# Performance work log

Hardware: AMD Instinct MI355X
Metric: run time of the kernel (lower is better)

The kernel has to match this reference:

```python
import jax, jax.numpy as jnp
import numpy as np

N_NODES = 100000
N_EDGES = 3200000
IN_DIM, HID, LAT = 81, 64, 32
BN_EPS = 1e-5


def setup_inputs() -> dict:
    key = jax.random.key(0)
    ks = jax.random.split(key, 16)
    def w(k, fan_in, fan_out):
        lim = 1.0 / np.sqrt(fan_in)
        return jax.random.uniform(k, (fan_in, fan_out), jnp.float32, -lim, lim)
    inp = {
        "x": jax.random.normal(ks[0], (N_NODES, IN_DIM), jnp.float32),
        "edge_index": jax.random.randint(ks[1], (2, N_EDGES), 0, N_NODES, jnp.int64),
        "W1": w(ks[2], IN_DIM, HID), "b1": jnp.zeros((HID,), jnp.float32),
        "g1": jnp.ones((HID,), jnp.float32), "beta1": jnp.zeros((HID,), jnp.float32),
        "W2": w(ks[3], HID, HID), "b2": jnp.zeros((HID,), jnp.float32),
        "g2": jnp.ones((HID,), jnp.float32), "beta2": jnp.zeros((HID,), jnp.float32),
        "Wmu": w(ks[4], HID, LAT), "bmu": jnp.zeros((LAT,), jnp.float32),
        "Wls": w(ks[5], HID, LAT), "bls": jnp.zeros((LAT,), jnp.float32),
    }
    return inp


def _gcn_norm(edge_index, num_nodes):
    # PyG gcn_norm: add self-loops, symmetric D^-1/2 A D^-1/2
    loop = jnp.arange(num_nodes, dtype=edge_index.dtype)
    src = jnp.concatenate([edge_index[0], loop])
    dst = jnp.concatenate([edge_index[1], loop])
    deg = jax.ops.segment_sum(jnp.ones_like(src, dtype=jnp.float32), dst,
                              num_segments=num_nodes)
    dis = jnp.where(deg > 0, jax.lax.rsqrt(jnp.maximum(deg, 1.0)), 0.0)
    norm = dis[src] * dis[dst]  # [E + N]
    return src, dst, norm


def _gcn_conv(x, W, b, src, dst, norm, num_nodes):
    h = x @ W                          # [N, out]
    msg = h[src] * norm[:, None]       # gather + scale
    out = jax.ops.segment_sum(msg, dst, num_segments=num_nodes)  # scatter-add
    return out + b


def _batchnorm(h, g, beta):
    m = h.mean(axis=0)
    v = h.var(axis=0)  # biased, as torch uses for normalization
    return (h - m) * jax.lax.rsqrt(v + BN_EPS) * g + beta


def reference(x, edge_index, W1, b1, g1, beta1, W2, b2, g2, beta2,
              Wmu, bmu, Wls, bls):
    n = x.shape[0]
    src, dst, norm = _gcn_norm(edge_index, n)
    h = _gcn_conv(x, W1, b1, src, dst, norm, n)
    h = jax.nn.relu(_batchnorm(h, g1, beta1))  # dropout = identity (eval)
    h = _gcn_conv(h, W2, b2, src, dst, norm, n)
    h = jax.nn.relu(_batchnorm(h, g2, beta2))
    mu = _gcn_conv(h, Wmu, bmu, src, dst, norm, n)
    logstd = _gcn_conv(h, Wls, bls, src, dst, norm, n)
    return (mu, logstd)
```

## Files before the change

### kernel.cpp

```cpp
#include <hip/hip_runtime.h>
#include <stdint.h>

#define N_NODES 100000
#define N_EDGES 3200000
#define IN_DIM  81
#define HID     64
#define LAT     32
#define BN_EPS  1e-5f
#define NBUCKET 391
#define EPB     8192
#define NBLK_E  391

__device__ __forceinline__ float bfu2f(unsigned short u) {
    return __uint_as_float(((uint32_t)u) << 16);
}
__device__ __forceinline__ unsigned short f2bfu(float f) {
    uint32_t x = __float_as_uint(f);
    return (unsigned short)((x + 0x7FFFu + ((x >> 16) & 1u)) >> 16);
}
__device__ __forceinline__ float loadf(const void* p, size_t i, int fp32) {
    if (fp32) return ((const float*)p)[i];
    return bfu2f(((const unsigned short*)p)[i]);
}
__device__ __forceinline__ int load_dst(const void* ei, int f64, long e) {
    if (f64) return (int)(((const long long*)ei)[(size_t)N_EDGES + e]);
    return ((const int*)ei)[(size_t)N_EDGES + e];
}
__device__ __forceinline__ int load_src(const void* ei, int f64, long e) {
    if (f64) return (int)(((const long long*)ei)[e]);
    return ((const int*)ei)[e];
}
__device__ __forceinline__ float bcast(float v, int k) {
    return __int_as_float(__builtin_amdgcn_readlane(__float_as_int(v), k));
}

__device__ __forceinline__ void fma8(float* acc, uint4 v, float d) {
    acc[0] = fmaf(__uint_as_float(v.x << 16), d, acc[0]);
    acc[1] = fmaf(__uint_as_float(v.x & 0xffff0000u), d, acc[1]);
    acc[2] = fmaf(__uint_as_float(v.y << 16), d, acc[2]);
    acc[3] = fmaf(__uint_as_float(v.y & 0xffff0000u), d, acc[3]);
    acc[4] = fmaf(__uint_as_float(v.z << 16), d, acc[4]);
    acc[5] = fmaf(__uint_as_float(v.z & 0xffff0000u), d, acc[5]);
    acc[6] = fmaf(__uint_as_float(v.w << 16), d, acc[6]);
    acc[7] = fmaf(__uint_as_float(v.w & 0xffff0000u), d, acc[7]);
}

__global__ void stamp_kernel(float* out, int n, float v) {
    int i = blockIdx.x * blockDim.x + threadIdx.x;
    if (i < n) out[i] = v;
}

__global__ void detect_all(const int* ei_raw,
                           const void* x, const void* W1, const void* b1,
                           const void* g1, const void* be1, const void* W2,
                           const void* b2, const void* g2, const void* be2,
                           const void* Wmu, const void* bmu, const void* Wls,
                           const void* bls, int* flags,
                           float* stats, int* bcnt) {
    int w = threadIdx.x >> 6;
    int lane = threadIdx.x & 63;
    if (w == 14) {
        for (int i = lane; i < 256; i += 64) stats[i] = 0.0f;
        return;
    }
    if (w == 15) {
        for (int i = lane; i < NBUCKET; i += 64) bcnt[i] = 0;
        return;
    }
    if (w == 13) {
        int acc = ei_raw[2 * lane * 11003 + 1] |
                  ei_raw[2 * (lane + 64) * 11003 + 1];
        unsigned long long b = __ballot(acc != 0);
        if (lane == 0) flags[0] = (b == 0ull) ? 1 : 0;
        return;
    }
    const void* bufs[13] = { x, W1, b1, g1, be1, W2, b2, g2, be2, Wmu, bmu, Wls, bls };
    const int   ns[13]   = { 512, 512, 64, 64, 64, 512, 64, 64, 64, 512, 32, 512, 32 };
    const unsigned short* u = (const unsigned short*)bufs[w];
    int n = ns[w];
    int evenZero = 0;
    bool oddNz = false, anyNz = false, big = false;
    for (int i = lane; i < n; i += 64) {
        unsigned short s = u[i];
        if (s) anyNz = true;
        if (i & 1) { if (s) oddNz = true; }
        else {
            if ((s & 0x7F80u) == 0x7F80u) big = true;
            else if (fabsf(bfu2f(s)) > 100.0f) big = true;
            if (s == 0) evenZero++;
        }
    }
    unsigned long long anyB = __ballot(anyNz);
    unsigned long long oddB = __ballot(oddNz);
    unsigned long long bigB = __ballot(big);
#pragma unroll
    for (int o = 1; o < 64; o <<= 1) evenZero += __shfl_xor(evenZero, o);
    if (lane == 0) {
        int fp32 = 0;
        if (anyB != 0ull) {
            if (bigB != 0ull) fp32 = 1;
            else if (evenZero >= n / 4 && oddB != 0ull) fp32 = 1;
        }
        flags[1 + w] = fp32;
    }
}

__global__ void convert_weights(const void* W1, const void* W2,
                                const void* Wmu, const void* Wls,
                                const void* b1, const void* b2,
                                const void* bmu, const void* bls,
                                const int* flags,
                                float* W1f, float* W2f, float* Wcatf,
                                float* b1f, float* b2f, float* bcatf) {
    int i = blockIdx.x * blockDim.x + threadIdx.x;
    if (i < IN_DIM * HID) { W1f[i] = loadf(W1, i, flags[2]); return; }
    i -= IN_DIM * HID;
    if (i < HID * HID) { W2f[i] = loadf(W2, i, flags[6]); return; }
    i -= HID * HID;
    if (i < HID * HID) {
        int k = i >> 6;
        int j = i & 63;
        if (j < LAT) Wcatf[i] = loadf(Wmu, (size_t)k * LAT + j, flags[10]);
        else         Wcatf[i] = loadf(Wls, (size_t)k * LAT + (j - LAT), flags[12]);
        return;
    }
    i -= HID * HID;
    if (i < HID) { b1f[i] = loadf(b1, i, flags[3]); return; }
    i -= HID;
    if (i < HID) { b2f[i] = loadf(b2, i, flags[7]); return; }
    i -= HID;
    if (i < HID) {
        if (i < LAT) bcatf[i] = loadf(bmu, i, flags[11]);
        else         bcatf[i] = loadf(bls, i - LAT, flags[13]);
    }
}

__global__ void bucket_hist(const void* ei, const int* flags, int* bcnt) {
    __shared__ int h[NBUCKET];
    for (int i = threadIdx.x; i < NBUCKET; i += 256) h[i] = 0;
    __syncthreads();
    int f64 = flags[0];
    long e0 = (long)blockIdx.x * EPB;
    for (int i = 0; i < EPB / 256; i++) {
        long e = e0 + i * 256 + threadIdx.x;
        if (e < N_EDGES) atomicAdd(&h[load_dst(ei, f64, e) >> 8], 1);
    }
    __syncthreads();
    for (int i = threadIdx.x; i < NBUCKET; i += 256)
        if (h[i]) atomicAdd(&bcnt[i], h[i]);
}

__global__ void bucket_scan(const int* bcnt, int* bbase, int* bcur, int* row_start) {
    __shared__ int sd[512];
    int t = threadIdx.x;
    int v0 = (t < NBUCKET) ? bcnt[t] : 0;
    int v1 = (t + 256 < NBUCKET) ? bcnt[t + 256] : 0;
    sd[t] = v0;
    sd[t + 256] = v1;
    __syncthreads();
    for (int off = 1; off < 256; off <<= 1) {
        int x = (t >= off) ? sd[t - off] : 0;
        __syncthreads();
        sd[t] += x;
        __syncthreads();
    }
    int low_total = sd[255];
    for (int off = 1; off < 256; off <<= 1) {
        int x = (t >= off) ? sd[256 + t - off] : 0;
        __syncthreads();
        sd[256 + t] += x;
        __syncthreads();
    }
    if (t < NBUCKET) {
        int excl = sd[t] - v0;
        bbase[t] = excl;
        bcur[t] = excl;
    }
    int j = 256 + t;
    if (j < NBUCKET) {
        int excl = sd[j] + low_total - v1;
        bbase[j] = excl;
        bcur[j] = excl;
    }
    if (t == 0) {
        bbase[NBUCKET] = N_EDGES;
        row_start[N_NODES] = N_EDGES;
    }
}

__global__ void bucket_scatter(const void* ei, const int* flags, int* bcur,
                               int* staged) {
    __shared__ int h[NBUCKET];
    __shared__ int lbase[NBUCKET];
    __shared__ int cnt[NBUCKET];
    for (int i = threadIdx.x; i < NBUCKET; i += 256) { h[i] = 0; cnt[i] = 0; }
    __syncthreads();
    int f64 = flags[0];
    long e0 = (long)blockIdx.x * EPB;
    for (int i = 0; i < EPB / 256; i++) {
        long e = e0 + i * 256 + threadIdx.x;
        if (e < N_EDGES) atomicAdd(&h[load_dst(ei, f64, e) >> 8], 1);
    }
    __syncthreads();
    for (int i = threadIdx.x; i < NBUCKET; i += 256)
        lbase[i] = h[i] ? atomicAdd(&bcur[i], h[i]) : 0;
    __syncthreads();
    for (int i = 0; i < EPB / 256; i++) {
        long e = e0 + i * 256 + threadIdx.x;
        if (e < N_EDGES) {
            int d = load_dst(ei, f64, e);
            int s = load_src(ei, f64, e);
            int b = d >> 8;
            int off = atomicAdd(&cnt[b], 1);
            staged[lbase[b] + off] = ((d & 255) << 17) | s;
        }
    }
}

__global__ void csr_build(const int* bbase, const int* staged, float* dis,
                          int* row_start, int* csr) {
    int b = blockIdx.x;
    int t = threadIdx.x;
    int n0 = b << 8;
    int nn = N_NODES - n0;
    if (nn > 256) nn = 256;
    int e0 = bbase[b];
    int e1 = bbase[b + 1];
    __shared__ int ldeg[256];
    __shared__ int lcur[256];
    __shared__ int sd[256];
    ldeg[t] = 0;
    __syncthreads();
    for (int i = e0 + t; i < e1; i += 256)
        atomicAdd(&ldeg[staged[i] >> 17], 1);
    __syncthreads();
    int v = ldeg[t];
    sd[t] = v;
    __syncthreads();
    for (int off = 1; off < 256; off <<= 1) {
        int x = (t >= off) ? sd[t - off] : 0;
        __syncthreads();
        sd[t] += x;
        __syncthreads();
    }
    int excl = sd[t] - v;
    if (t < nn) {
        dis[n0 + t] = rsqrtf((float)(v + 1));
        row_start[n0 + t] = e0 + excl;
    }
    lcur[t] = e0 + excl;
    __syncthreads();
    for (int i = e0 + t; i < e1; i += 256) {
        int rec = staged[i];
        int pos = atomicAdd(&lcur[rec >> 17], 1);
        csr[pos] = rec & 0x1FFFF;
    }
}

__global__ void gemm_l1(const void* X, const int* flags, const float* W,
                        unsigned short* T) {
    int wid = (blockIdx.x * blockDim.x + threadIdx.x) >> 6;
    int n0 = wid * 4;
    if (n0 >= N_NODES) return;
    int lane = threadIdx.x & 63;
    int fp = flags[1];
    float xa[4], xb[4];
#pragma unroll
    for (int nn = 0; nn < 4; nn++) {
        size_t base = (size_t)(n0 + nn) * IN_DIM;
        xa[nn] = loadf(X, base + lane, fp);
        xb[nn] = (lane < IN_DIM - 64) ? loadf(X, base + 64 + lane, fp) : 0.0f;
    }
    float acc[4] = { 0.0f, 0.0f, 0.0f, 0.0f };
    const float* Wp = W + lane;
#pragma unroll
    for (int k = 0; k < 64; k++) {
        float w = Wp[k * HID];
#pragma unroll
        for (int nn = 0; nn < 4; nn++)
            acc[nn] = fmaf(bcast(xa[nn], k), w, acc[nn]);
    }
#pragma unroll
    for (int k = 0; k < IN_DIM - 64; k++) {
        float w = Wp[(64 + k) * HID];
#pragma unroll
        for (int nn = 0; nn < 4; nn++)
            acc[nn] = fmaf(bcast(xb[nn], k), w, acc[nn]);
    }
#pragma unroll
    for (int nn = 0; nn < 4; nn++)
        T[(size_t)(n0 + nn) * HID + lane] = f2bfu(acc[nn]);
}

__global__ void gemm_bn(const float* F, const float* W,
                        const float* scale, const float* shift, unsigned short* T) {
    int wid = (blockIdx.x * blockDim.x + threadIdx.x) >> 6;
    int n0 = wid * 4;
    if (n0 >= N_NODES) return;
    int lane = threadIdx.x & 63;
    float sc = scale[lane];
    float sh = shift[lane];
    float a[4];
#pragma unroll
    for (int nn = 0; nn < 4; nn++) {
        float f = F[(size_t)(n0 + nn) * HID + lane];
        a[nn] = fmaxf(f * sc + sh, 0.0f);
    }
    float acc[4] = { 0.0f, 0.0f, 0.0f, 0.0f };
    const float* Wp = W + lane;
#pragma unroll
    for (int k = 0; k < HID; k++) {
        float w = Wp[k * HID];
#pragma unroll
        for (int nn = 0; nn < 4; nn++)
            acc[nn] = fmaf(bcast(a[nn], k), w, acc[nn]);
    }
#pragma unroll
    for (int nn = 0; nn < 4; nn++)
        T[(size_t)(n0 + nn) * HID + lane] = f2bfu(acc[nn]);
}

__global__ void agg_mid(const unsigned short* T, const int* row_start, const int* csr,
                        const float* dis, const float* bias, float* F) {
    int wid = (blockIdx.x * blockDim.x + threadIdx.x) >> 6;
    if (wid >= N_NODES) return;
    int lane = threadIdx.x & 63;
    int g = lane >> 3;
    int c = lane & 7;
    float dn = dis[wid];
    float acc[8];
#pragma unroll
    for (int k = 0; k < 8; k++) acc[k] = 0.0f;
    if (g == 0) {
        uint4 v = ((const uint4*)(T + (size_t)wid * HID))[c];
        fma8(acc, v, dn);
    }
    int s0 = row_start[wid];
    int s1 = row_start[wid + 1];
    for (int e = s0; e < s1; e += 32) {
        int i0 = e + g;
        int i1 = e + 8 + g;
        int i2 = e + 16 + g;
        int i3 = e + 24 + g;
        int m0 = i0 < s1, m1 = i1 < s1, m2 = i2 < s1, m3 = i3 < s1;
        int n0i = csr[m0 ? i0 : s0];
        int n1i = csr[m1 ? i1 : s0];
        int n2i = csr[m2 ? i2 : s0];
        int n3i = csr[m3 ? i3 : s0];
        float d0 = m0 ? dis[n0i] : 0.0f;
        float d1 = m1 ? dis[n1i] : 0.0f;
        float d2 = m2 ? dis[n2i] : 0.0f;
        float d3 = m3 ? dis[n3i] : 0.0f;
        uint4 v0 = ((const uint4*)(T + (size_t)n0i * HID))[c];
        uint4 v1 = ((const uint4*)(T + (size_t)n1i * HID))[c];
        uint4 v2 = ((const uint4*)(T + (size_t)n2i * HID))[c];
        uint4 v3 = ((const uint4*)(T + (size_t)n3i * HID))[c];
        fma8(acc, v0, d0);
        fma8(acc, v1, d1);
        fma8(acc, v2, d2);
        fma8(acc, v3, d3);
    }
#pragma unroll
    for (int k = 0; k < 8; k++) {
        float v = acc[k];
        v += __shfl_xor(v, 8);
        v += __shfl_xor(v, 16);
        v += __shfl_xor(v, 32);
        acc[k] = v;
    }
    if (g == 0) {
        const float4* bp = (const float4*)(bias + c * 8);
        float4 b0 = bp[0];
        float4 b1 = bp[1];
        float4 r0, r1;
        r0.x = b0.x + dn * acc[0];
        r0.y = b0.y + dn * acc[1];
        r0.z = b0.z + dn * acc[2];
        r0.w = b0.w + dn * acc[3];
        r1.x = b1.x + dn * acc[4];
        r1.y = b1.y + dn * acc[5];
        r1.z = b1.z + dn * acc[6];
        r1.w = b1.w + dn * acc[7];
        float4* o = (float4*)(F + (size_t)wid * HID + c * 8);
        o[0] = r0;
        o[1] = r1;
    }
}

__global__ void agg_out(const unsigned short* T, const int* row_start, const int* csr,
                        const float* dis, const float* bias, float* out) {
    int wid = (blockIdx.x * blockDim.x + threadIdx.x) >> 6;
    if (wid >= N_NODES) return;
    int lane = threadIdx.x & 63;
    int g = lane >> 3;
    int c = lane & 7;
    float dn = dis[wid];
    float acc[8];
#pragma unroll
    for (int k = 0; k < 8; k++) acc[k] = 0.0f;
    if (g == 0) {
        uint4 v = ((const uint4*)(T + (size_t)wid * HID))[c];
        fma8(acc, v, dn);
    }
    int s0 = row_start[wid];
    int s1 = row_start[wid + 1];
    for (int e = s0; e < s1; e += 32) {
        int i0 = e + g;
        int i1 = e + 8 + g;
        int i2 = e + 16 + g;
        int i3 = e + 24 + g;
        int m0 = i0 < s1, m1 = i1 < s1, m2 = i2 < s1, m3 = i3 < s1;
        int n0i = csr[m0 ? i0 : s0];
        int n1i = csr[m1 ? i1 : s0];
        int n2i = csr[m2 ? i2 : s0];
        int n3i = csr[m3 ? i3 : s0];
        float d0 = m0 ? dis[n0i] : 0.0f;
        float d1 = m1 ? dis[n1i] : 0.0f;
        float d2 = m2 ? dis[n2i] : 0.0f;
        float d3 = m3 ? dis[n3i] : 0.0f;
        uint4 v0 = ((const uint4*)(T + (size_t)n0i * HID))[c];
        uint4 v1 = ((const uint4*)(T + (size_t)n1i * HID))[c];
        uint4 v2 = ((const uint4*)(T + (size_t)n2i * HID))[c];
        uint4 v3 = ((const uint4*)(T + (size_t)n3i * HID))[c];
        fma8(acc, v0, d0);
        fma8(acc, v1, d1);
        fma8(acc, v2, d2);
        fma8(acc, v3, d3);
    }
#pragma unroll
    for (int k = 0; k < 8; k++) {
        float v = acc[k];
        v += __shfl_xor(v, 8);
        v += __shfl_xor(v, 16);
        v += __shfl_xor(v, 32);
        acc[k] = v;
    }
    if (g == 0) {
        const float4* bp = (const float4*)(bias + c * 8);
        float4 b0 = bp[0];
        float4 b1 = bp[1];
        float4 r0, r1;
        r0.x = b0.x + dn * acc[0];
        r0.y = b0.y + dn * acc[1];
        r0.z = b0.z + dn * acc[2];
        r0.w = b0.w + dn * acc[3];
        r1.x = b1.x + dn * acc[4];
        r1.y = b1.y + dn * acc[5];
        r1.z = b1.z + dn * acc[6];
        r1.w = b1.w + dn * acc[7];
        float4* o;
        if (c < 4)
            o = (float4*)(out + (size_t)wid * LAT + c * 8);
        else
            o = (float4*)(out + (size_t)N_NODES * LAT + (size_t)wid * LAT + (c - 4) * 8);
        o[0] = r0;
        o[1] = r1;
    }
}

__global__ void stats_kernel(const float* F, float* stats) {
    int lane = threadIdx.x & 63;
    int wv = threadIdx.x >> 6;
    float s = 0.0f;
    float q = 0.0f;
    for (int r = blockIdx.x * 4 + wv; r < N_NODES; r += gridDim.x * 4) {
        float v = F[(size_t)r * HID + lane];
        s += v;
        q += v * v;
    }
    __shared__ float ls[256];
    __shared__ float lq[256];
    ls[threadIdx.x] = s;
    lq[threadIdx.x] = q;
    __syncthreads();
    if (threadIdx.x < 64) {
        s = ls[threadIdx.x] + ls[64 + threadIdx.x] + ls[128 + threadIdx.x] + ls[192 + threadIdx.x];
        q = lq[threadIdx.x] + lq[64 + threadIdx.x] + lq[128 + threadIdx.x] + lq[192 + threadIdx.x];
        atomicAdd(&stats[lane], s);
        atomicAdd(&stats[64 + lane], q);
    }
}

__global__ void finalize_bn(const float* stats, const void* g, const void* beta,
                            const int* flags, int gflag, int bflag,
                            float* scale, float* shift) {
    int j = threadIdx.x;
    if (j >= HID) return;
    float inv_n = 1.0f / (float)N_NODES;
    float mean = stats[j] * inv_n;
    float var = stats[64 + j] * inv_n - mean * mean;
    float sc = loadf(g, j, flags[gflag]) * rsqrtf(var + BN_EPS);
    scale[j] = sc;
    shift[j] = loadf(beta, j, flags[bflag]) - mean * sc;
}

extern "C" void kernel_launch(void* const* d_in, const int* in_sizes, int n_in,
                              void* d_out, int out_size, void* d_ws, size_t ws_size,
                              hipStream_t stream) {
    (void)in_sizes;
    (void)n_in;
    const void* x   = d_in[0];
    const void* ei  = d_in[1];
    const void* W1  = d_in[2];
    const void* b1  = d_in[3];
    const void* g1  = d_in[4];
    const void* be1 = d_in[5];
    const void* W2  = d_in[6];
    const void* b2  = d_in[7];
    const void* g2  = d_in[8];
    const void* be2 = d_in[9];
    const void* Wmu = d_in[10];
    const void* bmu = d_in[11];
    const void* Wls = d_in[12];
    const void* bls = d_in[13];
    float* out = (float*)d_out;

    char* base = (char*)d_ws;
    size_t off = 0;
    int* staged = (int*)(base + off);
    off += (size_t)N_EDGES * 4;        off = (off + 511) & ~(size_t)511;
    int* csr = (int*)(base + off);
    off += (size_t)N_EDGES * 4;        off = (off + 511) & ~(size_t)511;
    unsigned short* T = (unsigned short*)(base + off);
    off += (size_t)N_NODES * HID * 2;  off = (off + 511) & ~(size_t)511;
    float* F = (float*)(base + off);
    off += (size_t)N_NODES * HID * 4;  off = (off + 511) & ~(size_t)511;
    float* dis = (float*)(base + off);
    off += (size_t)N_NODES * 4;        off = (off + 511) & ~(size_t)511;
    int* row_start = (int*)(base + off);
    off += (size_t)(N_NODES + 1) * 4;  off = (off + 511) & ~(size_t)511;
    int* bcnt = (int*)(base + off);
    off += NBUCKET * 4;                off = (off + 511) & ~(size_t)511;
    int* bbase = (int*)(base + off);
    off += (NBUCKET + 1) * 4;          off = (off + 511) & ~(size_t)511;
    int* bcur = (int*)(base + off);
    off += NBUCKET * 4;                off = (off + 511) & ~(size_t)511;
    int* flags = (int*)(base + off);
    off += 512;                        off = (off + 511) & ~(size_t)511;
    float* W1f = (float*)(base + off);
    off += (size_t)IN_DIM * HID * 4;   off = (off + 511) & ~(size_t)511;
    float* W2f = (float*)(base + off);
    off += (size_t)HID * HID * 4;      off = (off + 511) & ~(size_t)511;
    float* Wcatf = (float*)(base + off);
    off += (size_t)HID * HID * 4;      off = (off + 511) & ~(size_t)511;
    float* b1f = (float*)(base + off);
    off += HID * 4;                    off = (off + 511) & ~(size_t)511;
    float* b2f = (float*)(base + off);
    off += HID * 4;                    off = (off + 511) & ~(size_t)511;
    float* bcatf = (float*)(base + off);
    off += HID * 4;                    off = (off + 511) & ~(size_t)511;
    float* stats = (float*)(base + off);
    off += 256 * 4;                    off = (off + 511) & ~(size_t)511;
    float* scale1 = (float*)(base + off);
    off += HID * 4;                    off = (off + 511) & ~(size_t)511;
    float* shift1 = (float*)(base + off);
    off += HID * 4;                    off = (off + 511) & ~(size_t)511;
    float* scale2 = (float*)(base + off);
    off += HID * 4;                    off = (off + 511) & ~(size_t)511;
    float* shift2 = (float*)(base + off);
    off += HID * 4;

    const int BT = 256;
    int gW   = (N_NODES * 64 + BT - 1) / BT;
    int gG   = ((N_NODES / 4) * 64 + BT - 1) / BT;
    int gOut = (out_size + BT - 1) / BT;
    int gCv  = (IN_DIM * HID + 2 * HID * HID + 3 * HID + BT - 1) / BT;

    if (ws_size < off) {
        stamp_kernel<<<gOut, BT, 0, stream>>>(out, out_size, 6.8e37f);
        return;
    }

    detect_all<<<1, 1024, 0, stream>>>((const int*)ei, x, W1, b1, g1, be1, W2, b2,
                                       g2, be2, Wmu, bmu, Wls, bls, flags,
                                       stats, bcnt);
    convert_weights<<<gCv, BT, 0, stream>>>(W1, W2, Wmu, Wls, b1, b2, bmu, bls,
                                            flags, W1f, W2f, Wcatf, b1f, b2f, bcatf);

    bucket_hist<<<NBLK_E, BT, 0, stream>>>(ei, flags, bcnt);
    bucket_scan<<<1, BT, 0, stream>>>(bcnt, bbase, bcur, row_start);
    bucket_scatter<<<NBLK_E, BT, 0, stream>>>(ei, flags, bcur, staged);
    csr_build<<<NBUCKET, BT, 0, stream>>>(bbase, staged, dis, row_start, csr);

    gemm_l1<<<gG, BT, 0, stream>>>(x, flags, W1f, T);
    agg_mid<<<gW, BT, 0, stream>>>(T, row_start, csr, dis, b1f, F);
    stats_kernel<<<256, BT, 0, stream>>>(F, stats);
    finalize_bn<<<1, 64, 0, stream>>>(stats, g1, be1, flags, 4, 5, scale1, shift1);

    gemm_bn<<<gG, BT, 0, stream>>>(F, W2f, scale1, shift1, T);
    agg_mid<<<gW, BT, 0, stream>>>(T, row_start, csr, dis, b2f, F);
    stats_kernel<<<256, BT, 0, stream>>>(F, stats + 128);
    finalize_bn<<<1, 64, 0, stream>>>(stats + 128, g2, be2, flags, 8, 9, scale2, shift2);

    gemm_bn<<<gG, BT, 0, stream>>>(F, Wcatf, scale2, shift2, T);
    agg_out<<<gW, BT, 0, stream>>>(T, row_start, csr, dis, bcatf, out);
}
```

Before: 541.9 us.

## Fuse BN stats into aggregation and drop histogram/scan passes via fixed-capacity buckets

```diff
diff --git a/kernel.cpp b/kernel.cpp
--- a/kernel.cpp
+++ b/kernel.cpp
@@ -10,6 +10,8 @@
 #define NBUCKET 391
 #define EPB     8192
 #define NBLK_E  391
+#define BCAP    16384
+#define NSLICE  16
 
 __device__ __forceinline__ float bfu2f(unsigned short u) {
     return __uint_as_float(((uint32_t)u) << 16);
@@ -56,15 +58,15 @@
                            const void* b2, const void* g2, const void* be2,
                            const void* Wmu, const void* bmu, const void* Wls,
                            const void* bls, int* flags,
-                           float* stats, int* bcnt) {
+                           float* statsA, float* statsB, int* gcnt) {
     int w = threadIdx.x >> 6;
     int lane = threadIdx.x & 63;
     if (w == 14) {
-        for (int i = lane; i < 256; i += 64) stats[i] = 0.0f;
+        for (int i = lane; i < NSLICE * 128; i += 64) statsA[i] = 0.0f;
         return;
     }
     if (w == 15) {
-        for (int i = lane; i < NBUCKET; i += 64) bcnt[i] = 0;
+        for (int i = lane; i < NSLICE * 128; i += 64) statsB[i] = 0.0f;
         return;
     }
     if (w == 13) {
@@ -72,6 +74,7 @@
                   ei_raw[2 * (lane + 64) * 11003 + 1];
         unsigned long long b = __ballot(acc != 0);
         if (lane == 0) flags[0] = (b == 0ull) ? 1 : 0;
+        for (int i = lane; i < NBUCKET; i += 64) gcnt[i] = 0;
         return;
     }
     const void* bufs[13] = { x, W1, b1, g1, be1, W2, b2, g2, be2, Wmu, bmu, Wls, bls };
@@ -135,9 +138,12 @@
     }
 }
 
-__global__ void bucket_hist(const void* ei, const int* flags, int* bcnt) {
+__global__ void bucket_scatter(const void* ei, const int* flags, int* gcnt,
+                               int* staged) {
     __shared__ int h[NBUCKET];
-    for (int i = threadIdx.x; i < NBUCKET; i += 256) h[i] = 0;
+    __shared__ int lbase[NBUCKET];
+    __shared__ int lcnt[NBUCKET];
+    for (int i = threadIdx.x; i < NBUCKET; i += 256) { h[i] = 0; lcnt[i] = 0; }
     __syncthreads();
     int f64 = flags[0];
     long e0 = (long)blockIdx.x * EPB;
@@ -147,63 +153,7 @@
     }
     __syncthreads();
     for (int i = threadIdx.x; i < NBUCKET; i += 256)
-        if (h[i]) atomicAdd(&bcnt[i], h[i]);
-}
-
-__global__ void bucket_scan(const int* bcnt, int* bbase, int* bcur, int* row_start) {
-    __shared__ int sd[512];
-    int t = threadIdx.x;
-    int v0 = (t < NBUCKET) ? bcnt[t] : 0;
-    int v1 = (t + 256 < NBUCKET) ? bcnt[t + 256] : 0;
-    sd[t] = v0;
-    sd[t + 256] = v1;
-    __syncthreads();
-    for (int off = 1; off < 256; off <<= 1) {
-        int x = (t >= off) ? sd[t - off] : 0;
-        __syncthreads();
-        sd[t] += x;
-        __syncthreads();
-    }
-    int low_total = sd[255];
-    for (int off = 1; off < 256; off <<= 1) {
-        int x = (t >= off) ? sd[256 + t - off] : 0;
-        __syncthreads();
-        sd[256 + t] += x;
-        __syncthreads();
-    }
-    if (t < NBUCKET) {
-        int excl = sd[t] - v0;
-        bbase[t] = excl;
-        bcur[t] = excl;
-    }
-    int j = 256 + t;
-    if (j < NBUCKET) {
-        int excl = sd[j] + low_total - v1;
-        bbase[j] = excl;
-        bcur[j] = excl;
-    }
-    if (t == 0) {
-        bbase[NBUCKET] = N_EDGES;
-        row_start[N_NODES] = N_EDGES;
-    }
-}
-
-__global__ void bucket_scatter(const void* ei, const int* flags, int* bcur,
-                               int* staged) {
-    __shared__ int h[NBUCKET];
-    __shared__ int lbase[NBUCKET];
-    __shared__ int cnt[NBUCKET];
-    for (int i = threadIdx.x; i < NBUCKET; i += 256) { h[i] = 0; cnt[i] = 0; }
-    __syncthreads();
-    int f64 = flags[0];
-    long e0 = (long)blockIdx.x * EPB;
-    for (int i = 0; i < EPB / 256; i++) {
-        long e = e0 + i * 256 + threadIdx.x;
-        if (e < N_EDGES) atomicAdd(&h[load_dst(ei, f64, e) >> 8], 1);
-    }
-    __syncthreads();
-    for (int i = threadIdx.x; i < NBUCKET; i += 256)
-        lbase[i] = h[i] ? atomicAdd(&bcur[i], h[i]) : 0;
+        lbase[i] = h[i] ? atomicAdd(&gcnt[i], h[i]) : 0;
     __syncthreads();
     for (int i = 0; i < EPB / 256; i++) {
         long e = e0 + i * 256 + threadIdx.x;
@@ -211,28 +161,38 @@
             int d = load_dst(ei, f64, e);
             int s = load_src(ei, f64, e);
             int b = d >> 8;
-            int off = atomicAdd(&cnt[b], 1);
-            staged[lbase[b] + off] = ((d & 255) << 17) | s;
-        }
-    }
-}
-
-__global__ void csr_build(const int* bbase, const int* staged, float* dis,
+            int off = atomicAdd(&lcnt[b], 1);
+            staged[(b << 14) + lbase[b] + off] = ((d & 255) << 17) | s;
+        }
+    }
+}
+
+__global__ void csr_build(const int* gcnt, const int* staged, float* dis,
                           int* row_start, int* csr) {
     int b = blockIdx.x;
     int t = threadIdx.x;
     int n0 = b << 8;
     int nn = N_NODES - n0;
     if (nn > 256) nn = 256;
-    int e0 = bbase[b];
-    int e1 = bbase[b + 1];
+    __shared__ int sd[256];
     __shared__ int ldeg[256];
     __shared__ int lcur[256];
-    __shared__ int sd[256];
+    int p = 0;
+    for (int i = t; i < b; i += 256) p += gcnt[i];
+    sd[t] = p;
+    __syncthreads();
+    for (int off = 128; off >= 1; off >>= 1) {
+        if (t < off) sd[t] += sd[t + off];
+        __syncthreads();
+    }
+    int e0 = sd[0];
+    int cntb = gcnt[b];
+    __syncthreads();
     ldeg[t] = 0;
     __syncthreads();
-    for (int i = e0 + t; i < e1; i += 256)
-        atomicAdd(&ldeg[staged[i] >> 17], 1);
+    const int* sb = staged + ((size_t)b << 14);
+    for (int i = t; i < cntb; i += 256)
+        atomicAdd(&ldeg[sb[i] >> 17], 1);
     __syncthreads();
     int v = ldeg[t];
     sd[t] = v;
@@ -250,11 +210,12 @@
     }
     lcur[t] = e0 + excl;
     __syncthreads();
-    for (int i = e0 + t; i < e1; i += 256) {
-        int rec = staged[i];
+    for (int i = t; i < cntb; i += 256) {
+        int rec = sb[i];
         int pos = atomicAdd(&lcur[rec >> 17], 1);
         csr[pos] = rec & 0x1FFFF;
     }
+    if (b == NBUCKET - 1 && t == 0) row_start[N_NODES] = e0 + cntb;
 }
 
 __global__ void gemm_l1(const void* X, const int* flags, const float* W,
@@ -292,14 +253,24 @@
         T[(size_t)(n0 + nn) * HID + lane] = f2bfu(acc[nn]);
 }
 
-__global__ void gemm_bn(const float* F, const float* W,
-                        const float* scale, const float* shift, unsigned short* T) {
+__global__ void gemm_bn(const float* F, const float* W, const float* stats,
+                        const void* gw, const void* bw, const int* flags,
+                        int gf, int bf, unsigned short* T) {
     int wid = (blockIdx.x * blockDim.x + threadIdx.x) >> 6;
     int n0 = wid * 4;
     if (n0 >= N_NODES) return;
     int lane = threadIdx.x & 63;
-    float sc = scale[lane];
-    float sh = shift[lane];
+    float s = 0.0f, q = 0.0f;
+#pragma unroll
+    for (int sl = 0; sl < NSLICE; sl++) {
+        s += stats[sl * 128 + lane];
+        q += stats[sl * 128 + 64 + lane];
+    }
+    const float inv_n = 1.0f / (float)N_NODES;
+    float mean = s * inv_n;
+    float var = q * inv_n - mean * mean;
+    float sc = loadf(gw, lane, flags[gf]) * rsqrtf(var + BN_EPS);
+    float sh = loadf(bw, lane, flags[bf]) - mean * sc;
     float a[4];
 #pragma unroll
     for (int nn = 0; nn < 4; nn++) {
@@ -321,7 +292,94 @@
 }
 
 __global__ void agg_mid(const unsigned short* T, const int* row_start, const int* csr,
-                        const float* dis, const float* bias, float* F) {
+                        const float* dis, const float* bias, float* F, float* stats) {
+    __shared__ float ls[64];
+    __shared__ float lq[64];
+    if (threadIdx.x < 64) { ls[threadIdx.x] = 0.0f; lq[threadIdx.x] = 0.0f; }
+    __syncthreads();
+    int wid = (blockIdx.x * blockDim.x + threadIdx.x) >> 6;
+    int lane = threadIdx.x & 63;
+    int g = lane >> 3;
+    int c = lane & 7;
+    if (wid < N_NODES) {
+        float dn = dis[wid];
+        float acc[8];
+#pragma unroll
+        for (int k = 0; k < 8; k++) acc[k] = 0.0f;
+        if (g == 0) {
+            uint4 v = ((const uint4*)(T + (size_t)wid * HID))[c];
+            fma8(acc, v, dn);
+        }
+        int s0 = row_start[wid];
+        int s1 = row_start[wid + 1];
+        for (int e = s0; e < s1; e += 32) {
+            int i0 = e + g;
+            int i1 = e + 8 + g;
+            int i2 = e + 16 + g;
+            int i3 = e + 24 + g;
+            int m0 = i0 < s1, m1 = i1 < s1, m2 = i2 < s1, m3 = i3 < s1;
+            int n0i = csr[m0 ? i0 : s0];
+            int n1i = csr[m1 ? i1 : s0];
+            int n2i = csr[m2 ? i2 : s0];
+            int n3i = csr[m3 ? i3 : s0];
+            float d0 = m0 ? dis[n0i] : 0.0f;
+            float d1 = m1 ? dis[n1i] : 0.0f;
+            float d2 = m2 ? dis[n2i] : 0.0f;
+            float d3 = m3 ? dis[n3i] : 0.0f;
+            uint4 v0 = ((const uint4*)(T + (size_t)n0i * HID))[c];
+            uint4 v1 = ((const uint4*)(T + (size_t)n1i * HID))[c];
+            uint4 v2 = ((const uint4*)(T + (size_t)n2i * HID))[c];
+            uint4 v3 = ((const uint4*)(T + (size_t)n3i * HID))[c];
+            fma8(acc, v0, d0);
+            fma8(acc, v1, d1);
+            fma8(acc, v2, d2);
+            fma8(acc, v3, d3);
+        }
+#pragma unroll
+        for (int k = 0; k < 8; k++) {
+            float v = acc[k];
+            v += __shfl_xor(v, 8);
+            v += __shfl_xor(v, 16);
+            v += __shfl_xor(v, 32);
+            acc[k] = v;
+        }
+        if (g == 0) {
+            const float4* bp = (const float4*)(bias + c * 8);
+            float4 b0 = bp[0];
+            float4 b1 = bp[1];
+            float4 r0, r1;
+            r0.x = b0.x + dn * acc[0];
+            r0.y = b0.y + dn * acc[1];
+            r0.z = b0.z + dn * acc[2];
+            r0.w = b0.w + dn * acc[3];
+            r1.x = b1.x + dn * acc[4];
+            r1.y = b1.y + dn * acc[5];
+            r1.z = b1.z + dn * acc[6];
+            r1.w = b1.w + dn * acc[7];
+            float4* o = (float4*)(F + (size_t)wid * HID + c * 8);
+            o[0] = r0;
+            o[1] = r1;
+            int f0 = c * 8;
+            atomicAdd(&ls[f0 + 0], r0.x); atomicAdd(&lq[f0 + 0], r0.x * r0.x);
+            atomicAdd(&ls[f0 + 1], r0.y); atomicAdd(&lq[f0 + 1], r0.y * r0.y);
+            atomicAdd(&ls[f0 + 2], r0.z); atomicAdd(&lq[f0 + 2], r0.z * r0.z);
+            atomicAdd(&ls[f0 + 3], r0.w); atomicAdd(&lq[f0 + 3], r0.w * r0.w);
+            atomicAdd(&ls[f0 + 4], r1.x); atomicAdd(&lq[f0 + 4], r1.x * r1.x);
+            atomicAdd(&ls[f0 + 5], r1.y); atomicAdd(&lq[f0 + 5], r1.y * r1.y);
+            atomicAdd(&ls[f0 + 6], r1.z); atomicAdd(&lq[f0 + 6], r1.z * r1.z);
+            atomicAdd(&ls[f0 + 7], r1.w); atomicAdd(&lq[f0 + 7], r1.w * r1.w);
+        }
+    }
+    __syncthreads();
+    if (threadIdx.x < 64) {
+        int sl = blockIdx.x & (NSLICE - 1);
+        atomicAdd(&stats[sl * 128 + threadIdx.x], ls[threadIdx.x]);
+        atomicAdd(&stats[sl * 128 + 64 + threadIdx.x], lq[threadIdx.x]);
+    }
+}
+
+__global__ void agg_out(const unsigned short* T, const int* row_start, const int* csr,
+                        const float* dis, const float* bias, float* out) {
     int wid = (blockIdx.x * blockDim.x + threadIdx.x) >> 6;
     if (wid >= N_NODES) return;
     int lane = threadIdx.x & 63;
@@ -381,73 +439,6 @@
         r1.y = b1.y + dn * acc[5];
         r1.z = b1.z + dn * acc[6];
         r1.w = b1.w + dn * acc[7];
-        float4* o = (float4*)(F + (size_t)wid * HID + c * 8);
-        o[0] = r0;
-        o[1] = r1;
-    }
-}
-
-__global__ void agg_out(const unsigned short* T, const int* row_start, const int* csr,
-                        const float* dis, const float* bias, float* out) {
-    int wid = (blockIdx.x * blockDim.x + threadIdx.x) >> 6;
-    if (wid >= N_NODES) return;
-    int lane = threadIdx.x & 63;
-    int g = lane >> 3;
-    int c = lane & 7;
-    float dn = dis[wid];
-    float acc[8];
-#pragma unroll
-    for (int k = 0; k < 8; k++) acc[k] = 0.0f;
-    if (g == 0) {
-        uint4 v = ((const uint4*)(T + (size_t)wid * HID))[c];
-        fma8(acc, v, dn);
-    }
-    int s0 = row_start[wid];
-    int s1 = row_start[wid + 1];
-    for (int e = s0; e < s1; e += 32) {
-        int i0 = e + g;
-        int i1 = e + 8 + g;
-        int i2 = e + 16 + g;
-        int i3 = e + 24 + g;
-        int m0 = i0 < s1, m1 = i1 < s1, m2 = i2 < s1, m3 = i3 < s1;
-        int n0i = csr[m0 ? i0 : s0];
-        int n1i = csr[m1 ? i1 : s0];
-        int n2i = csr[m2 ? i2 : s0];
-        int n3i = csr[m3 ? i3 : s0];
-        float d0 = m0 ? dis[n0i] : 0.0f;
-        float d1 = m1 ? dis[n1i] : 0.0f;
-        float d2 = m2 ? dis[n2i] : 0.0f;
-        float d3 = m3 ? dis[n3i] : 0.0f;
-        uint4 v0 = ((const uint4*)(T + (size_t)n0i * HID))[c];
-        uint4 v1 = ((const uint4*)(T + (size_t)n1i * HID))[c];
-        uint4 v2 = ((const uint4*)(T + (size_t)n2i * HID))[c];
-        uint4 v3 = ((const uint4*)(T + (size_t)n3i * HID))[c];
-        fma8(acc, v0, d0);
-        fma8(acc, v1, d1);
-        fma8(acc, v2, d2);
-        fma8(acc, v3, d3);
-    }
-#pragma unroll
-    for (int k = 0; k < 8; k++) {
-        float v = acc[k];
-        v += __shfl_xor(v, 8);
-        v += __shfl_xor(v, 16);
-        v += __shfl_xor(v, 32);
-        acc[k] = v;
-    }
-    if (g == 0) {
-        const float4* bp = (const float4*)(bias + c * 8);
-        float4 b0 = bp[0];
-        float4 b1 = bp[1];
-        float4 r0, r1;
-        r0.x = b0.x + dn * acc[0];
-        r0.y = b0.y + dn * acc[1];
-        r0.z = b0.z + dn * acc[2];
-        r0.w = b0.w + dn * acc[3];
-        r1.x = b1.x + dn * acc[4];
-        r1.y = b1.y + dn * acc[5];
-        r1.z = b1.z + dn * acc[6];
-        r1.w = b1.w + dn * acc[7];
         float4* o;
         if (c < 4)
             o = (float4*)(out + (size_t)wid * LAT + c * 8);
@@ -456,42 +447,6 @@
         o[0] = r0;
         o[1] = r1;
     }
-}
-
-__global__ void stats_kernel(const float* F, float* stats) {
-    int lane = threadIdx.x & 63;
-    int wv = threadIdx.x >> 6;
-    float s = 0.0f;
-    float q = 0.0f;
-    for (int r = blockIdx.x * 4 + wv; r < N_NODES; r += gridDim.x * 4) {
-        float v = F[(size_t)r * HID + lane];
-        s += v;
-        q += v * v;
-    }
-    __shared__ float ls[256];
-    __shared__ float lq[256];
-    ls[threadIdx.x] = s;
-    lq[threadIdx.x] = q;
-    __syncthreads();
-    if (threadIdx.x < 64) {
-        s = ls[threadIdx.x] + ls[64 + threadIdx.x] + ls[128 + threadIdx.x] + ls[192 + threadIdx.x];
-        q = lq[threadIdx.x] + lq[64 + threadIdx.x] + lq[128 + threadIdx.x] + lq[192 + threadIdx.x];
-        atomicAdd(&stats[lane], s);
-        atomicAdd(&stats[64 + lane], q);
-    }
-}
-
-__global__ void finalize_bn(const float* stats, const void* g, const void* beta,
-                            const int* flags, int gflag, int bflag,
-                            float* scale, float* shift) {
-    int j = threadIdx.x;
-    if (j >= HID) return;
-    float inv_n = 1.0f / (float)N_NODES;
-    float mean = stats[j] * inv_n;
-    float var = stats[64 + j] * inv_n - mean * mean;
-    float sc = loadf(g, j, flags[gflag]) * rsqrtf(var + BN_EPS);
-    scale[j] = sc;
-    shift[j] = loadf(beta, j, flags[bflag]) - mean * sc;
 }
 
 extern "C" void kernel_launch(void* const* d_in, const int* in_sizes, int n_in,
@@ -517,23 +472,20 @@
 
     char* base = (char*)d_ws;
     size_t off = 0;
-    int* staged = (int*)(base + off);
-    off += (size_t)N_EDGES * 4;        off = (off + 511) & ~(size_t)511;
+    int*   staged = (int*)(base + off);
+    float* F      = (float*)(base + off);
+    size_t uni = (size_t)NBUCKET * BCAP * 4;
+    if ((size_t)N_NODES * HID * 4 > uni) uni = (size_t)N_NODES * HID * 4;
+    off += uni;                        off = (off + 511) & ~(size_t)511;
     int* csr = (int*)(base + off);
     off += (size_t)N_EDGES * 4;        off = (off + 511) & ~(size_t)511;
     unsigned short* T = (unsigned short*)(base + off);
     off += (size_t)N_NODES * HID * 2;  off = (off + 511) & ~(size_t)511;
-    float* F = (float*)(base + off);
-    off += (size_t)N_NODES * HID * 4;  off = (off + 511) & ~(size_t)511;
     float* dis = (float*)(base + off);
     off += (size_t)N_NODES * 4;        off = (off + 511) & ~(size_t)511;
     int* row_start = (int*)(base + off);
     off += (size_t)(N_NODES + 1) * 4;  off = (off + 511) & ~(size_t)511;
-    int* bcnt = (int*)(base + off);
-    off += NBUCKET * 4;                off = (off + 511) & ~(size_t)511;
-    int* bbase = (int*)(base + off);
-    off += (NBUCKET + 1) * 4;          off = (off + 511) & ~(size_t)511;
-    int* bcur = (int*)(base + off);
+    int* gcnt = (int*)(base + off);
     off += NBUCKET * 4;                off = (off + 511) & ~(size_t)511;
     int* flags = (int*)(base + off);
     off += 512;                        off = (off + 511) & ~(size_t)511;
@@ -549,16 +501,10 @@
     off += HID * 4;                    off = (off + 511) & ~(size_t)511;
     float* bcatf = (float*)(base + off);
     off += HID * 4;                    off = (off + 511) & ~(size_t)511;
-    float* stats = (float*)(base + off);
-    off += 256 * 4;                    off = (off + 511) & ~(size_t)511;
-    float* scale1 = (float*)(base + off);
-    off += HID * 4;                    off = (off + 511) & ~(size_t)511;
-    float* shift1 = (float*)(base + off);
-    off += HID * 4;                    off = (off + 511) & ~(size_t)511;
-    float* scale2 = (float*)(base + off);
-    off += HID * 4;                    off = (off + 511) & ~(size_t)511;
-    float* shift2 = (float*)(base + off);
-    off += HID * 4;
+    float* statsA = (float*)(base + off);
+    off += NSLICE * 128 * 4;           off = (off + 511) & ~(size_t)511;
+    float* statsB = (float*)(base + off);
+    off += NSLICE * 128 * 4;           off = (off + 511) & ~(size_t)511;
 
     const int BT = 256;
     int gW   = (N_NODES * 64 + BT - 1) / BT;
@@ -573,25 +519,19 @@
 
     detect_all<<<1, 1024, 0, stream>>>((const int*)ei, x, W1, b1, g1, be1, W2, b2,
                                        g2, be2, Wmu, bmu, Wls, bls, flags,
-                                       stats, bcnt);
+                                       statsA, statsB, gcnt);
     convert_weights<<<gCv, BT, 0, stream>>>(W1, W2, Wmu, Wls, b1, b2, bmu, bls,
                                             flags, W1f, W2f, Wcatf, b1f, b2f, bcatf);
 
-    bucket_hist<<<NBLK_E, BT, 0, stream>>>(ei, flags, bcnt);
-    bucket_scan<<<1, BT, 0, stream>>>(bcnt, bbase, bcur, row_start);
-    bucket_scatter<<<NBLK_E, BT, 0, stream>>>(ei, flags, bcur, staged);
-    csr_build<<<NBUCKET, BT, 0, stream>>>(bbase, staged, dis, row_start, csr);
+    bucket_scatter<<<NBLK_E, BT, 0, stream>>>(ei, flags, gcnt, staged);
+    csr_build<<<NBUCKET, BT, 0, stream>>>(gcnt, staged, dis, row_start, csr);
 
     gemm_l1<<<gG, BT, 0, stream>>>(x, flags, W1f, T);
-    agg_mid<<<gW, BT, 0, stream>>>(T, row_start, csr, dis, b1f, F);
-    stats_kernel<<<256, BT, 0, stream>>>(F, stats);
-    finalize_bn<<<1, 64, 0, stream>>>(stats, g1, be1, flags, 4, 5, scale1, shift1);
-
-    gemm_bn<<<gG, BT, 0, stream>>>(F, W2f, scale1, shift1, T);
-    agg_mid<<<gW, BT, 0, stream>>>(T, row_start, csr, dis, b2f, F);
-    stats_kernel<<<256, BT, 0, stream>>>(F, stats + 128);
-    finalize_bn<<<1, 64, 0, stream>>>(stats + 128, g2, be2, flags, 8, 9, scale2, shift2);
-
-    gemm_bn<<<gG, BT, 0, stream>>>(F, Wcatf, scale2, shift2, T);
+    agg_mid<<<gW, BT, 0, stream>>>(T, row_start, csr, dis, b1f, F, statsA);
+
+    gemm_bn<<<gG, BT, 0, stream>>>(F, W2f, statsA, g1, be1, flags, 4, 5, T);
+    agg_mid<<<gW, BT, 0, stream>>>(T, row_start, csr, dis, b2f, F, statsB);
+
+    gemm_bn<<<gG, BT, 0, stream>>>(F, Wcatf, statsB, g2, be2, flags, 8, 9, T);
     agg_out<<<gW, BT, 0, stream>>>(T, row_start, csr, dis, bcatf, out);
 }
```

Result: slower. 571.6 us (+5.5%).
